# Kernel tuning notes

Measured on AMD Instinct MI355X. Metric: run time of the kernel, lower is better.

Reference implementation:

```python
import jax, jax.numpy as jnp
import numpy as np

B, T, E, H, L = 64, 512, 768, 256, 9


def setup_inputs() -> dict:
    key = jax.random.key(0)
    ks = jax.random.split(key, 16)
    k = 1.0 / np.sqrt(H)
    u = lambda i, shape: jax.random.uniform(ks[i], shape, jnp.float32, -k, k)
    embeddings = jax.random.normal(ks[0], (B, T, E), jnp.float32)
    lengths = jax.random.randint(ks[1], (B,), T // 2, T + 1)
    attention_mask = jnp.arange(T)[None, :] < lengths[:, None]  # [B,T] bool, mask[:,0] all True
    labels = jax.random.randint(ks[2], (B, T), 0, L).astype(jnp.int32)
    return dict(
        embeddings=embeddings,
        W_ih_f=u(3, (4 * H, E)), W_hh_f=u(4, (4 * H, H)), b_f=u(5, (4 * H,)),
        W_ih_b=u(6, (4 * H, E)), W_hh_b=u(7, (4 * H, H)), b_b=u(8, (4 * H,)),
        W_lin=u(9, (L, 2 * H)), b_lin=u(10, (L,)),
        start_trans=0.1 * jax.random.normal(ks[11], (L,), jnp.float32),
        end_trans=0.1 * jax.random.normal(ks[12], (L,), jnp.float32),
        transitions=0.1 * jax.random.normal(ks[13], (L, L), jnp.float32),
        attention_mask=attention_mask,
        labels=labels,
    )


def _lstm_dir(x_tm, W_ih, W_hh, b, reverse):
    # x_tm: [T,B,E] -> hidden states [T,B,H]; PyTorch gate order i,f,g,o
    xg = jnp.einsum('tbe,ge->tbg', x_tm, W_ih) + b  # [T,B,4H]
    Hh = W_hh.shape[1]

    def step(carry, g_in):
        h, c = carry
        g = g_in + h @ W_hh.T
        i, f, gg, o = jnp.split(g, 4, axis=-1)
        c = jax.nn.sigmoid(f) * c + jax.nn.sigmoid(i) * jnp.tanh(gg)
        h = jax.nn.sigmoid(o) * jnp.tanh(c)
        return (h, c), h

    Bn = x_tm.shape[1]
    init = (jnp.zeros((Bn, Hh), x_tm.dtype), jnp.zeros((Bn, Hh), x_tm.dtype))
    _, hs = jax.lax.scan(step, init, xg, reverse=reverse)
    return hs


def reference(embeddings, W_ih_f, W_hh_f, b_f, W_ih_b, W_hh_b, b_b,
              W_lin, b_lin, start_trans, end_trans, transitions,
              attention_mask, labels):
    x_tm = embeddings.transpose(1, 0, 2)  # [T,B,E]
    h_f = _lstm_dir(x_tm, W_ih_f, W_hh_f, b_f, False)
    h_b = _lstm_dir(x_tm, W_ih_b, W_hh_b, b_b, True)
    feats = jnp.concatenate([h_f, h_b], axis=-1)  # [T,B,2H]
    em = jnp.einsum('tbh,lh->tbl', feats, W_lin) + b_lin  # [T,B,L]

    mask = attention_mask.astype(em.dtype).T  # [T,B]
    tags = labels.T  # [T,B]
    Bn = em.shape[1]
    bidx = jnp.arange(Bn)

    # --- numerator: score of gold path (torchcrf _compute_score) ---
    num = start_trans[tags[0]] + em[0, bidx, tags[0]]
    trans_sc = transitions[tags[:-1], tags[1:]]                                  # [T-1,B]
    em_sc = jnp.take_along_axis(em[1:], tags[1:, :, None], axis=2)[..., 0]       # [T-1,B]
    num = num + jnp.sum((trans_sc + em_sc) * mask[1:], axis=0)
    last_idx = attention_mask.astype(jnp.int32).sum(axis=1) - 1                  # [B]
    last_tags = labels[bidx, last_idx]
    num = num + end_trans[last_tags]

    # --- denominator: log partition via forward algorithm (lax.scan) ---
    score0 = start_trans + em[0]  # [B,L]

    def step(score, inp):
        em_t, m_t = inp
        nxt = jax.nn.logsumexp(score[:, :, None] + transitions[None] + em_t[:, None, :], axis=1)
        return jnp.where(m_t[:, None] > 0, nxt, score), None

    score, _ = jax.lax.scan(step, score0, (em[1:], mask[1:]))
    logZ = jax.nn.logsumexp(score + end_trans, axis=1)  # [B]

    # loss = -crf(emissions, labels, mask, reduction='mean')
    return jnp.mean(logZ - num)
```

## Files before the change

kernel.cpp:

```cpp
#include <hip/hip_runtime.h>
#include <hip/hip_bf16.h>
#include <cstdint>
#include <cstddef>


typedef __attribute__((ext_vector_type(8))) short short8;
typedef __attribute__((ext_vector_type(4))) float floatx4;
typedef __attribute__((ext_vector_type(2))) float floatx2;
typedef __attribute__((ext_vector_type(8))) int v8i;
typedef unsigned short ushort_t;
typedef unsigned char uchar_t;
typedef unsigned int uint_t;
typedef unsigned long long ull_t;

#define NB   64
#define NT   512
#define NE   768
#define NH   256
#define NL   9
#define NG   1024
#define NCC  2048
#define HPAD 272

__device__ inline float asf(uint_t u) {
    union { uint_t i; float f; } v; v.i = u; return v.f;
}
__device__ inline ushort_t f2b(float f) {
    union { float f; uint_t i; } v; v.f = f;
    uint_t r = (v.i + 0x7FFFu + ((v.i >> 16) & 1u)) >> 16;
    return (ushort_t)r;
}

__device__ inline void g2lds16(const void* g, void* l) {
    __builtin_amdgcn_global_load_lds(
        (const __attribute__((address_space(1))) uint_t*)g,
        (__attribute__((address_space(3))) uint_t*)l, 16, 0, 0);
}

__global__ void conv_x(const float* __restrict__ emb, ushort_t* __restrict__ xbf) {
    int id = blockIdx.x * blockDim.x + threadIdx.x;
    int t  = id / (NB * (NE / 4));
    int rm = id - t * (NB * (NE / 4));
    int b  = rm / (NE / 4);
    int e4 = rm - b * (NE / 4);
    const float4 v = *(const float4*)(emb + ((size_t)b * NT + t) * NE + e4 * 4);
    ushort_t o[4] = { f2b(v.x), f2b(v.y), f2b(v.z), f2b(v.w) };
    *(uint2*)(xbf + ((size_t)t * NB + b) * NE + e4 * 4) = *(const uint2*)o;
}

__global__ void conv_w(const float* __restrict__ Wihf, const float* __restrict__ Wihb,
                       const float* __restrict__ Whhf, const float* __restrict__ Whhb,
                       const float* __restrict__ bf,   const float* __restrict__ bb,
                       ushort_t* __restrict__ wcat, uchar_t* __restrict__ whh8,
                       float* __restrict__ bias) {
    int idx = blockIdx.x * blockDim.x + threadIdx.x;
    const int NW1 = NCC * NE;
    const int NW2 = NCC * NH / 2;
    const float SC1 = 1.4426950408889634f;
    const float SC2 = 2.8853900817779268f;
    if (idx < NW1) {
        int rowp = idx / NE, col = idx - rowp * NE;
        int d = rowp >> 10, rr = rowp & 1023;
        int hu = rr >> 2, gate = rr & 3;
        float sc = (gate == 2) ? SC2 : SC1;
        const float* W = d ? Wihb : Wihf;
        wcat[idx] = f2b(W[(size_t)(gate * NH + hu) * NE + col] * sc);
    } else if (idx < NW1 + NW2) {
        int j = idx - NW1;
        int rowp = j >> 7, kp = (j & 127) * 2;
        int d = rowp >> 10, rr = rowp & 1023;
        int hu = rr >> 2, gate = rr & 3;
        float sc = (gate == 2) ? SC2 : SC1;
        const float* W = d ? Whhb : Whhf;
        float f0 = W[(size_t)(gate * NH + hu) * NH + kp] * sc;
        float f1 = W[(size_t)(gate * NH + hu) * NH + kp + 1] * sc;
        uint_t pk = __builtin_amdgcn_cvt_pk_fp8_f32(f0, f1, 0, false);
        *(ushort_t*)(whh8 + (size_t)rowp * NH + kp) = (ushort_t)(pk & 0xFFFF);
    } else if (idx < NW1 + NW2 + NCC) {
        int rowp = idx - NW1 - NW2;
        int d = rowp >> 10, rr = rowp & 1023;
        int hu = rr >> 2, gate = rr & 3;
        float sc = (gate == 2) ? SC2 : SC1;
        bias[rowp] = (d ? bb : bf)[gate * NH + hu] * sc;
    }
}

__global__ __launch_bounds__(256) void gemm_xg(const ushort_t* __restrict__ A,
                                               const ushort_t* __restrict__ W,
                                               const float* __restrict__ bias,
                                               ushort_t* __restrict__ C) {
    __shared__ __align__(16) ushort_t As[128 * 64];
    __shared__ __align__(16) ushort_t Bs[128 * 64];
    const int tid = threadIdx.x;
    const int wave = tid >> 6, lane = tid & 63;
    const int q = lane >> 4, m16 = lane & 15;
    const int wm = wave & 1, wn = wave >> 1;
    const int m0 = blockIdx.y * 128, n0 = blockIdx.x * 128;

    floatx4 acc[4][4];
    #pragma unroll
    for (int i = 0; i < 4; ++i)
        #pragma unroll
        for (int j = 0; j < 4; ++j) acc[i][j] = (floatx4){0.f, 0.f, 0.f, 0.f};

    for (int kt = 0; kt < NE / 64; ++kt) {
        __syncthreads();
        #pragma unroll
        for (int it = 0; it < 4; ++it) {
            int chunk = tid + it * 256;
            int row = chunk >> 3, kc = chunk & 7;
            int kcs = kc ^ (row & 7);
            g2lds16(A + (size_t)(m0 + row) * NE + kt * 64 + kcs * 8,
                    (uchar_t*)As + chunk * 16);
            g2lds16(W + (size_t)(n0 + row) * NE + kt * 64 + kcs * 8,
                    (uchar_t*)Bs + chunk * 16);
        }
        __syncthreads();
        #pragma unroll
        for (int ks = 0; ks < 2; ++ks) {
            short8 af[4], bfr[4];
            #pragma unroll
            for (int mt = 0; mt < 4; ++mt) {
                int row = wm * 64 + mt * 16 + m16;
                int slot = (ks * 4 + q) ^ (m16 & 7);
                af[mt] = *(const short8*)((const uchar_t*)As + row * 128 + slot * 16);
            }
            #pragma unroll
            for (int nt = 0; nt < 4; ++nt) {
                int row = wn * 64 + nt * 16 + m16;
                int slot = (ks * 4 + q) ^ (m16 & 7);
                bfr[nt] = *(const short8*)((const uchar_t*)Bs + row * 128 + slot * 16);
            }
            #pragma unroll
            for (int mt = 0; mt < 4; ++mt)
                #pragma unroll
                for (int nt = 0; nt < 4; ++nt)
                    acc[mt][nt] = __builtin_amdgcn_mfma_f32_16x16x32_bf16(
                        af[mt], bfr[nt], acc[mt][nt], 0, 0, 0);
        }
    }
    float bcol[4];
    #pragma unroll
    for (int nt = 0; nt < 4; ++nt) bcol[nt] = bias[n0 + wn * 64 + nt * 16 + m16];
    #pragma unroll
    for (int mt = 0; mt < 4; ++mt)
        #pragma unroll
        for (int nt = 0; nt < 4; ++nt) {
            int gn = n0 + wn * 64 + nt * 16 + m16;
            #pragma unroll
            for (int r = 0; r < 4; ++r) {
                int gm = m0 + wm * 64 + mt * 16 + q * 4 + r;
                C[(size_t)gm * NCC + gn] = f2b(acc[mt][nt][r] + bcol[nt]);
            }
        }
}

__device__ inline uchar_t lstm_gate(floatx4 a, ull_t xr, float& cc) {
    uint_t lo = (uint_t)xr, hi = (uint_t)(xr >> 32);
    float pi = a[0] + asf(lo << 16);
    float pf = a[1] + asf(lo & 0xffff0000u);
    float pg = a[2] + asf(hi << 16);
    float po = a[3] + asf(hi & 0xffff0000u);
    float ei = __builtin_amdgcn_exp2f(-fmaxf(pi, -40.f));
    float ef = __builtin_amdgcn_exp2f(-fmaxf(pf, -40.f));
    float eo = __builtin_amdgcn_exp2f(-fmaxf(po, -40.f));
    float ug = __builtin_amdgcn_exp2f(fminf(pg, 40.f));
    float A  = 1.f + ei, Bv = 1.f + ug, C = 1.f + ef;
    float AB  = A * Bv;
    float num = fmaf(Bv - 2.f, C, cc * AB);
    float cn  = num * __builtin_amdgcn_rcpf(C * AB);
    cc = cn;
    float uc = __builtin_amdgcn_exp2f(fminf(cn * 2.8853900817779268f, 40.f));
    float h  = (uc - 1.f) * __builtin_amdgcn_rcpf((uc + 1.f) * (1.f + eo));
    uint_t pk = __builtin_amdgcn_cvt_pk_fp8_f32(h, h, 0, false);
    return (uchar_t)(pk & 0xFF);
}

__global__ __launch_bounds__(512, 2) void lstm_k(const ushort_t* __restrict__ xg,
                                                 const uchar_t* __restrict__ whh8,
                                                 uchar_t* __restrict__ hhist8) {
    const int d  = blockIdx.x >> 5;
    const int bg = blockIdx.x & 31;
    const int tid = threadIdx.x;
    const int w = tid >> 6, lane = tid & 63;
    const int q = lane >> 4, m16 = lane & 15;
    const int hu   = w * 32 + (lane >> 1);
    const int bloc = lane & 1;
    const int blg  = bg * 2 + bloc;

    __shared__ uchar_t hb8[2][16 * HPAD];
    __shared__ float   accT[2048];
    for (int i = tid; i < 2 * 16 * HPAD; i += 512) ((uchar_t*)hb8)[i] = 0;

    const uchar_t* wp = whh8 + (size_t)(d * NG + w * 128) * NH;
    v8i wreg[8][2];
    #pragma unroll
    for (int mt = 0; mt < 8; ++mt)
        #pragma unroll
        for (int kh = 0; kh < 2; ++kh)
            wreg[mt][kh] = *(const v8i*)(wp + (size_t)(mt * 16 + m16) * NH + kh * 128 + q * 32);
    #pragma unroll
    for (int mt = 0; mt < 8; ++mt)
        #pragma unroll
        for (int kh = 0; kh < 2; ++kh)
            asm volatile("" : "+a"(wreg[mt][kh]));

    float cc = 0.f;
    __syncthreads();

    const int scl = 0x7f7f7f7f;
    const ushort_t* xb_ = xg + (size_t)d * NG + hu * 4;

    ull_t xw, xwn;
    {
        const int t0 = d ? (NT - 1) : 0;
        xw = *(const ull_t*)(xb_ + (size_t)(t0 * NB + blg) * NCC);
    }
    floatx4 z4 = (floatx4){0.f, 0.f, 0.f, 0.f};
    asm volatile("" : "+v"(z4));

    #pragma unroll 1
    for (int s = 0; s < NT; ++s) {
        const int t = d ? (NT - 1 - s) : s;

        if (s + 1 < NT) {
            const int tn = d ? (NT - 2 - s) : (s + 1);
            xwn = *(const ull_t*)(xb_ + (size_t)(tn * NB + blg) * NCC);
        }

        const uchar_t* hrow = &hb8[s & 1][m16 * HPAD];
        v8i hf0 = *(const v8i*)(hrow + q * 32);
        v8i hf1 = *(const v8i*)(hrow + 128 + q * 32);

        floatx4 acc[8];
        #pragma unroll
        for (int mt = 0; mt < 8; ++mt)
            acc[mt] = __builtin_amdgcn_mfma_scale_f32_16x16x128_f8f6f4(
                wreg[mt][0], hf0, z4, 0, 0, 0, scl, 0, scl);
        #pragma unroll
        for (int mt = 0; mt < 8; ++mt)
            acc[mt] = __builtin_amdgcn_mfma_scale_f32_16x16x128_f8f6f4(
                wreg[mt][1], hf1, acc[mt], 0, 0, 0, scl, 0, scl);

        if (m16 < 2) {
            #pragma unroll
            for (int mt = 0; mt < 8; ++mt) {
                int hu_w = w * 32 + mt * 4 + q;
                *(floatx4*)((uchar_t*)accT + (size_t)hu_w * 32 + m16 * 16) = acc[mt];
            }
        }
        __syncthreads();

        floatx4 a = *(const floatx4*)((const uchar_t*)accT + (size_t)hu * 32 + bloc * 16);
        uchar_t hv = lstm_gate(a, xw, cc);
        hb8[(s + 1) & 1][bloc * HPAD + hu] = hv;

        xw = xwn;
        __syncthreads();

        if (tid < 64) {
            int b_ = tid >> 5, off = (tid & 31) * 8;
            ull_t v = *(const ull_t*)(&hb8[(s + 1) & 1][b_ * HPAD + off]);
            *(ull_t*)(hhist8 + ((size_t)(d * NT + t) * NB + bg * 2 + b_) * NH + off) = v;
        }
    }
}

__global__ void em_k(const uchar_t* __restrict__ hhist8, const float* __restrict__ Wlin,
                     const float* __restrict__ blin, float* __restrict__ em) {
    const int t = blockIdx.x;
    const int tid = threadIdx.x;
    __shared__ float Ws[NL * 520];
    for (int idx = tid; idx < NL * 2 * NH; idx += 576) {
        int l = idx >> 9, k = idx & 511;
        Ws[l * 520 + k] = Wlin[l * 2 * NH + k];
    }
    __syncthreads();
    const int b = tid / NL, l = tid - b * NL;
    const uchar_t* hf = hhist8 + ((size_t)t * NB + b) * NH;
    const uchar_t* hb = hhist8 + ((size_t)(NT + t) * NB + b) * NH;
    float acc = blin[l];
    #pragma unroll 4
    for (int kc = 0; kc < NH / 4; ++kc) {
        uint_t u = *(const uint_t*)(hf + kc * 4);
        floatx2 p0 = __builtin_amdgcn_cvt_pk_f32_fp8(u, false);
        floatx2 p1 = __builtin_amdgcn_cvt_pk_f32_fp8(u, true);
        acc += p0.x * Ws[l * 520 + kc * 4]     + p0.y * Ws[l * 520 + kc * 4 + 1]
             + p1.x * Ws[l * 520 + kc * 4 + 2] + p1.y * Ws[l * 520 + kc * 4 + 3];
    }
    #pragma unroll 4
    for (int kc = 0; kc < NH / 4; ++kc) {
        uint_t u = *(const uint_t*)(hb + kc * 4);
        floatx2 p0 = __builtin_amdgcn_cvt_pk_f32_fp8(u, false);
        floatx2 p1 = __builtin_amdgcn_cvt_pk_f32_fp8(u, true);
        acc += p0.x * Ws[l * 520 + NH + kc * 4]     + p0.y * Ws[l * 520 + NH + kc * 4 + 1]
             + p1.x * Ws[l * 520 + NH + kc * 4 + 2] + p1.y * Ws[l * 520 + NH + kc * 4 + 3];
    }
    em[((size_t)t * NB + b) * NL + l] = acc;
}

__global__ void num_k(const float* __restrict__ em, const int* __restrict__ mask,
                      const int* __restrict__ labels, const float* __restrict__ start,
                      const float* __restrict__ endt, const float* __restrict__ trans,
                      float* __restrict__ numbuf) {
    const int b = blockIdx.x;
    const int lane = threadIdx.x;
    int cntm = 0;
    for (int t = lane; t < NT; t += 64) cntm += (mask[b * NT + t] != 0);
    #pragma unroll
    for (int off = 32; off > 0; off >>= 1) cntm += __shfl_down(cntm, off);
    const int len = __shfl(cntm, 0);

    float part = 0.f;
    for (int t = lane; t < NT; t += 64) {
        if (t >= 1 && t < len) {
            int tp = labels[b * NT + t - 1];
            int tg = labels[b * NT + t];
            part += trans[tp * NL + tg] + em[((size_t)t * NB + b) * NL + tg];
        }
    }
    #pragma unroll
    for (int off = 32; off > 0; off >>= 1) part += __shfl_down(part, off);
    if (lane == 0) {
        int tag0 = labels[b * NT];
        numbuf[b] = part + start[tag0] + em[(size_t)b * NL + tag0]
                  + endt[labels[b * NT + len - 1]];
    }
}

__global__ void crf_k(const float* __restrict__ em, const int* __restrict__ mask,
                      const float* __restrict__ start, const float* __restrict__ endt,
                      const float* __restrict__ trans, const float* __restrict__ numbuf,
                      float* __restrict__ diff) {
    const int b = blockIdx.x;
    const int lane = threadIdx.x;
    int cnt = 0;
    for (int t = lane; t < NT; t += 64) cnt += (mask[b * NT + t] != 0);
    #pragma unroll
    for (int off = 32; off > 0; off >>= 1) cnt += __shfl_down(cnt, off);
    const int len = __shfl(cnt, 0);

    float tcol[NL];
    #pragma unroll
    for (int i = 0; i < NL; ++i) tcol[i] = (lane < NL) ? trans[i * NL + lane] : 0.f;
    float endv = (lane < NL) ? endt[lane] : 0.f;
    float score = (lane < NL) ? start[lane] + em[(size_t)b * NL + lane] : -1e30f;

    for (int t = 1; t < len; ++t) {
        float emv = (lane < NL) ? em[((size_t)t * NB + b) * NL + lane] : 0.f;
        float sv[NL];
        #pragma unroll
        for (int i = 0; i < NL; ++i) sv[i] = __shfl(score, i) + tcol[i];
        float m = sv[0];
        #pragma unroll
        for (int i = 1; i < NL; ++i) m = fmaxf(m, sv[i]);
        float sum = 0.f;
        #pragma unroll
        for (int i = 0; i < NL; ++i) sum += __expf(sv[i] - m);
        float nxt = m + __logf(sum) + emv;
        if (lane < NL) score = nxt;
    }
    float v = (lane < NL) ? score + endv : -1e30f;
    float m = -1e30f;
    float sv[NL];
    #pragma unroll
    for (int i = 0; i < NL; ++i) { sv[i] = __shfl(v, i); m = fmaxf(m, sv[i]); }
    float sum = 0.f;
    #pragma unroll
    for (int i = 0; i < NL; ++i) sum += __expf(sv[i] - m);
    float logZ = m + __logf(sum);
    if (lane == 0) diff[b] = logZ - numbuf[b];
}

__global__ void final_k(const float* __restrict__ diff, float* __restrict__ out) {
    float v = diff[threadIdx.x];
    #pragma unroll
    for (int off = 32; off > 0; off >>= 1) v += __shfl_down(v, off);
    if (threadIdx.x == 0) out[0] = v * (1.0f / NB);
}

extern "C" void kernel_launch(void* const* d_in, const int* in_sizes, int n_in,
                              void* d_out, int out_size, void* d_ws, size_t ws_size,
                              hipStream_t stream) {
    const float* emb   = (const float*)d_in[0];
    const float* Wihf  = (const float*)d_in[1];
    const float* Whhf  = (const float*)d_in[2];
    const float* bf    = (const float*)d_in[3];
    const float* Wihb  = (const float*)d_in[4];
    const float* Whhb  = (const float*)d_in[5];
    const float* bb    = (const float*)d_in[6];
    const float* Wlin  = (const float*)d_in[7];
    const float* blin  = (const float*)d_in[8];
    const float* start = (const float*)d_in[9];
    const float* endt  = (const float*)d_in[10];
    const float* trans = (const float*)d_in[11];
    const int*   mask  = (const int*)d_in[12];
    const int*   labels= (const int*)d_in[13];

    char* ws = (char*)d_ws;
    ushort_t* xbf   = (ushort_t*)(ws + 0);
    ushort_t* wcat  = (ushort_t*)(ws + 50331648);
    uchar_t*  whh8  = (uchar_t*) (ws + 53477376);
    float*    bias  = (float*)   (ws + 54001664);
    ushort_t* xg    = (ushort_t*)(ws + 54009856);
    uchar_t*  hh8   = (uchar_t*) (ws + 188227584);
    float*    em    = (float*)   (ws + 205004800);
    float*    numb  = (float*)   (ws + 206184448);
    float*    diff  = (float*)   (ws + 206184704);

    conv_x<<<NT * NB * (NE / 4) / 256, 256, 0, stream>>>(emb, xbf);
    conv_w<<<(NCC * NE + NCC * NH / 2 + NCC) / 256, 256, 0, stream>>>(
        Wihf, Wihb, Whhf, Whhb, bf, bb, wcat, whh8, bias);
    gemm_xg<<<dim3(NCC / 128, NT * NB / 128), 256, 0, stream>>>(xbf, wcat, bias, xg);
    lstm_k<<<64, 512, 0, stream>>>(xg, whh8, hh8);
    em_k<<<NT, 576, 0, stream>>>(hh8, Wlin, blin, em);
    num_k<<<NB, 64, 0, stream>>>(em, mask, labels, start, endt, trans, numb);
    crf_k<<<NB, 64, 0, stream>>>(em, mask, start, endt, trans, numb, diff);
    final_k<<<1, 64, 0, stream>>>(diff, (float*)d_out);
}
```

Baseline: 1.060 ms.

## Switch input projection GEMM to FP8 scaled MFMA with swizzled block order

Converts the embeddings and input weights to FP8 instead of bf16 and runs the input-projection GEMM with the 16x16x128 FP8 scaled MFMA. This halves the bytes read for activations and weights and doubles the K depth per instruction, cutting the number of K iterations. Block indices are also remapped so neighbouring blocks share rows, which should improve L2 reuse. The cost is accuracy: the input projection now uses 8-bit mantissa-poor values for unnormalized embeddings.

```diff
diff --git a/kernel.cpp b/kernel.cpp
--- a/kernel.cpp
+++ b/kernel.cpp
@@ -37,34 +37,38 @@
         (__attribute__((address_space(3))) uint_t*)l, 16, 0, 0);
 }
 
-__global__ void conv_x(const float* __restrict__ emb, ushort_t* __restrict__ xbf) {
+__global__ void conv_x(const float* __restrict__ emb, uchar_t* __restrict__ xbf8) {
     int id = blockIdx.x * blockDim.x + threadIdx.x;
     int t  = id / (NB * (NE / 4));
     int rm = id - t * (NB * (NE / 4));
     int b  = rm / (NE / 4);
     int e4 = rm - b * (NE / 4);
     const float4 v = *(const float4*)(emb + ((size_t)b * NT + t) * NE + e4 * 4);
-    ushort_t o[4] = { f2b(v.x), f2b(v.y), f2b(v.z), f2b(v.w) };
-    *(uint2*)(xbf + ((size_t)t * NB + b) * NE + e4 * 4) = *(const uint2*)o;
+    uint_t p = __builtin_amdgcn_cvt_pk_fp8_f32(v.x, v.y, 0, false);
+    p = __builtin_amdgcn_cvt_pk_fp8_f32(v.z, v.w, p, true);
+    *(uint_t*)(xbf8 + ((size_t)t * NB + b) * NE + e4 * 4) = p;
 }
 
 __global__ void conv_w(const float* __restrict__ Wihf, const float* __restrict__ Wihb,
                        const float* __restrict__ Whhf, const float* __restrict__ Whhb,
                        const float* __restrict__ bf,   const float* __restrict__ bb,
-                       ushort_t* __restrict__ wcat, uchar_t* __restrict__ whh8,
+                       uchar_t* __restrict__ wcat8, uchar_t* __restrict__ whh8,
                        float* __restrict__ bias) {
     int idx = blockIdx.x * blockDim.x + threadIdx.x;
-    const int NW1 = NCC * NE;
+    const int NW1 = NCC * NE / 2;
     const int NW2 = NCC * NH / 2;
     const float SC1 = 1.4426950408889634f;
     const float SC2 = 2.8853900817779268f;
     if (idx < NW1) {
-        int rowp = idx / NE, col = idx - rowp * NE;
+        int rowp = idx / (NE / 2), cp = (idx - rowp * (NE / 2)) * 2;
         int d = rowp >> 10, rr = rowp & 1023;
         int hu = rr >> 2, gate = rr & 3;
         float sc = (gate == 2) ? SC2 : SC1;
         const float* W = d ? Wihb : Wihf;
-        wcat[idx] = f2b(W[(size_t)(gate * NH + hu) * NE + col] * sc);
+        float f0 = W[(size_t)(gate * NH + hu) * NE + cp] * sc;
+        float f1 = W[(size_t)(gate * NH + hu) * NE + cp + 1] * sc;
+        uint_t pk = __builtin_amdgcn_cvt_pk_fp8_f32(f0, f1, 0, false);
+        *(ushort_t*)(wcat8 + (size_t)rowp * NE + cp) = (ushort_t)(pk & 0xFFFF);
     } else if (idx < NW1 + NW2) {
         int j = idx - NW1;
         int rowp = j >> 7, kp = (j & 127) * 2;
@@ -85,17 +89,19 @@
     }
 }
 
-__global__ __launch_bounds__(256) void gemm_xg(const ushort_t* __restrict__ A,
-                                               const ushort_t* __restrict__ W,
+__global__ __launch_bounds__(256) void gemm_xg(const uchar_t* __restrict__ A,
+                                               const uchar_t* __restrict__ W,
                                                const float* __restrict__ bias,
                                                ushort_t* __restrict__ C) {
-    __shared__ __align__(16) ushort_t As[128 * 64];
-    __shared__ __align__(16) ushort_t Bs[128 * 64];
+    __shared__ __align__(16) uchar_t As[128 * 128];
+    __shared__ __align__(16) uchar_t Bs[128 * 128];
     const int tid = threadIdx.x;
     const int wave = tid >> 6, lane = tid & 63;
     const int q = lane >> 4, m16 = lane & 15;
     const int wm = wave & 1, wn = wave >> 1;
-    const int m0 = blockIdx.y * 128, n0 = blockIdx.x * 128;
+    int flat = blockIdx.y * 16 + blockIdx.x;
+    int fs = (flat & 7) * 512 + (flat >> 3);
+    const int m0 = (fs >> 4) * 128, n0 = (fs & 15) * 128;
 
     floatx4 acc[4][4];
     #pragma unroll
@@ -103,41 +109,47 @@
         #pragma unroll
         for (int j = 0; j < 4; ++j) acc[i][j] = (floatx4){0.f, 0.f, 0.f, 0.f};
 
-    for (int kt = 0; kt < NE / 64; ++kt) {
+    const int scl = 0x7f7f7f7f;
+    union V8U { v8i v; uint4 u[2]; };
+
+    for (int kt = 0; kt < NE / 128; ++kt) {
         __syncthreads();
         #pragma unroll
         for (int it = 0; it < 4; ++it) {
             int chunk = tid + it * 256;
-            int row = chunk >> 3, kc = chunk & 7;
-            int kcs = kc ^ (row & 7);
-            g2lds16(A + (size_t)(m0 + row) * NE + kt * 64 + kcs * 8,
-                    (uchar_t*)As + chunk * 16);
-            g2lds16(W + (size_t)(n0 + row) * NE + kt * 64 + kcs * 8,
-                    (uchar_t*)Bs + chunk * 16);
+            int row = chunk >> 3, sn = chunk & 7;
+            int ss = sn ^ (row & 7);
+            g2lds16(A + (size_t)(m0 + row) * NE + kt * 128 + ss * 16,
+                    As + chunk * 16);
+            g2lds16(W + (size_t)(n0 + row) * NE + kt * 128 + ss * 16,
+                    Bs + chunk * 16);
         }
         __syncthreads();
-        #pragma unroll
-        for (int ks = 0; ks < 2; ++ks) {
-            short8 af[4], bfr[4];
+
+        v8i af[4], bfr[4];
+        const int s0 = (2 * q) ^ (m16 & 7), s1 = (2 * q + 1) ^ (m16 & 7);
+        #pragma unroll
+        for (int mt = 0; mt < 4; ++mt) {
+            int row = wm * 64 + mt * 16 + m16;
+            V8U t;
+            t.u[0] = *(const uint4*)(As + row * 128 + s0 * 16);
+            t.u[1] = *(const uint4*)(As + row * 128 + s1 * 16);
+            af[mt] = t.v;
+        }
+        #pragma unroll
+        for (int nt = 0; nt < 4; ++nt) {
+            int row = wn * 64 + nt * 16 + m16;
+            V8U t;
+            t.u[0] = *(const uint4*)(Bs + row * 128 + s0 * 16);
+            t.u[1] = *(const uint4*)(Bs + row * 128 + s1 * 16);
+            bfr[nt] = t.v;
+        }
+        #pragma unroll
+        for (int mt = 0; mt < 4; ++mt)
             #pragma unroll
-            for (int mt = 0; mt < 4; ++mt) {
-                int row = wm * 64 + mt * 16 + m16;
-                int slot = (ks * 4 + q) ^ (m16 & 7);
-                af[mt] = *(const short8*)((const uchar_t*)As + row * 128 + slot * 16);
-            }
-            #pragma unroll
-            for (int nt = 0; nt < 4; ++nt) {
-                int row = wn * 64 + nt * 16 + m16;
-                int slot = (ks * 4 + q) ^ (m16 & 7);
-                bfr[nt] = *(const short8*)((const uchar_t*)Bs + row * 128 + slot * 16);
-            }
-            #pragma unroll
-            for (int mt = 0; mt < 4; ++mt)
-                #pragma unroll
-                for (int nt = 0; nt < 4; ++nt)
-                    acc[mt][nt] = __builtin_amdgcn_mfma_f32_16x16x32_bf16(
-                        af[mt], bfr[nt], acc[mt][nt], 0, 0, 0);
-        }
+            for (int nt = 0; nt < 4; ++nt)
+                acc[mt][nt] = __builtin_amdgcn_mfma_scale_f32_16x16x128_f8f6f4(
+                    af[mt], bfr[nt], acc[mt][nt], 0, 0, 0, scl, 0, scl);
     }
     float bcol[4];
     #pragma unroll
@@ -398,8 +410,8 @@
     const int*   labels= (const int*)d_in[13];
 
     char* ws = (char*)d_ws;
-    ushort_t* xbf   = (ushort_t*)(ws + 0);
-    ushort_t* wcat  = (ushort_t*)(ws + 50331648);
+    uchar_t*  xbf8  = (uchar_t*) (ws + 0);
+    uchar_t*  wcat8 = (uchar_t*) (ws + 50331648);
     uchar_t*  whh8  = (uchar_t*) (ws + 53477376);
     float*    bias  = (float*)   (ws + 54001664);
     ushort_t* xg    = (ushort_t*)(ws + 54009856);
@@ -408,10 +420,10 @@
     float*    numb  = (float*)   (ws + 206184448);
     float*    diff  = (float*)   (ws + 206184704);
 
-    conv_x<<<NT * NB * (NE / 4) / 256, 256, 0, stream>>>(emb, xbf);
-    conv_w<<<(NCC * NE + NCC * NH / 2 + NCC) / 256, 256, 0, stream>>>(
-        Wihf, Wihb, Whhf, Whhb, bf, bb, wcat, whh8, bias);
-    gemm_xg<<<dim3(NCC / 128, NT * NB / 128), 256, 0, stream>>>(xbf, wcat, bias, xg);
+    conv_x<<<NT * NB * (NE / 4) / 256, 256, 0, stream>>>(emb, xbf8);
+    conv_w<<<(NCC * NE / 2 + NCC * NH / 2 + NCC) / 256, 256, 0, stream>>>(
+        Wihf, Wihb, Whhf, Whhb, bf, bb, wcat8, whh8, bias);
+    gemm_xg<<<dim3(NCC / 128, NT * NB / 128), 256, 0, stream>>>(xbf8, wcat8, bias, xg);
     lstm_k<<<64, 512, 0, stream>>>(xg, whh8, hh8);
     em_k<<<NT, 576, 0, stream>>>(hh8, Wlin, blin, em);
     num_k<<<NB, 64, 0, stream>>>(em, mask, labels, start, endt, trans, numb);
```

New measurement: 990.1 us. 6.5% less time.
